# Kernel tuning notes

Hardware: AMD Instinct MI355X
Metric: run time of the kernel (lower is better)

The kernel has to match this reference:

```python
import jax, jax.numpy as jnp
import numpy as np

B, T, D, L = 64, 512, 400, 25
H = D // 2  # per-direction LSTM hidden


def setup_inputs():
    key = jax.random.key(0)
    ks = jax.random.split(key, 16)
    s = 0.1
    lengths = jax.random.randint(ks[0], (B,), T // 2, T + 1)
    mask = (jnp.arange(T)[None, :] < lengths[:, None]).astype(jnp.float32)
    labels = (jax.random.randint(ks[1], (B, T), 1, L) * mask.astype(jnp.int32)).astype(jnp.int32)

    def n(k, shape):
        return jax.random.normal(k, shape, jnp.float32) * s

    return {
        "input_embed": jax.random.normal(ks[2], (B, T, D), jnp.float32),
        "mask": mask,
        "labels": labels,
        "Wih_f": n(ks[3], (4 * H, D)), "Whh_f": n(ks[4], (4 * H, H)),
        "bih_f": n(ks[5], (4 * H,)), "bhh_f": n(ks[6], (4 * H,)),
        "Wih_b": n(ks[7], (4 * H, D)), "Whh_b": n(ks[8], (4 * H, H)),
        "bih_b": n(ks[9], (4 * H,)), "bhh_b": n(ks[10], (4 * H,)),
        "Wl": n(ks[11], (L, D)), "bl": n(ks[12], (L,)),
        "trans": n(ks[13], (L, L)), "start": n(ks[14], (L,)), "end": n(ks[15], (L,)),
    }


def _lstm_dir(x_tbd, m_tb1, Wih, Whh, bih, bhh, reverse):
    # Masked LSTM scan == pack_padded semantics: state frozen past sequence end.
    Bn = x_tbd.shape[1]
    h0 = jnp.zeros((Bn, H), x_tbd.dtype)

    def step(carry, inp):
        h, c = carry
        x, m = inp
        g = x @ Wih.T + h @ Whh.T + (bih + bhh)
        i, f, gg, o = jnp.split(g, 4, axis=-1)  # PyTorch gate order i,f,g,o
        i, f, o = jax.nn.sigmoid(i), jax.nn.sigmoid(f), jax.nn.sigmoid(o)
        c_new = f * c + i * jnp.tanh(gg)
        h_new = o * jnp.tanh(c_new)
        h = m * h_new + (1.0 - m) * h
        c = m * c_new + (1.0 - m) * c
        return (h, c), h

    _, hs = jax.lax.scan(step, (h0, h0), (x_tbd, m_tb1), reverse=reverse)
    return hs  # [T,B,H]


def _emissions(input_embed, mask, params):
    (Wih_f, Whh_f, bih_f, bhh_f, Wih_b, Whh_b, bih_b, bhh_b, Wl, bl) = params
    x = jnp.transpose(input_embed, (1, 0, 2))    # [T,B,D]
    m = jnp.transpose(mask, (1, 0))[:, :, None]  # [T,B,1]
    hf = _lstm_dir(x, m, Wih_f, Whh_f, bih_f, bhh_f, False)
    hb = _lstm_dir(x, m, Wih_b, Whh_b, bih_b, bhh_b, True)
    h = jnp.concatenate([hf, hb], axis=-1) * m   # pad positions zeroed like pad_packed_sequence
    e = (h @ Wl.T + bl) * m                      # `out *= mask.unsqueeze(-1)`
    return jnp.transpose(e, (1, 0, 2))           # [B,T,L]


def _crf_llh(e, labels, mask, trans, start, end):
    # numerator (gold path score)
    em = jnp.take_along_axis(e, labels[..., None], axis=-1)[..., 0]  # [B,T]
    tr = trans[labels[:, :-1], labels[:, 1:]]                        # [B,T-1]
    last = (jnp.sum(mask, axis=1) - 1.0).astype(jnp.int32)
    y_last = jnp.take_along_axis(labels, last[:, None], axis=1)[:, 0]
    num = start[labels[:, 0]] + em[:, 0] \
        + jnp.sum(mask[:, 1:] * (em[:, 1:] + tr), axis=1) + end[y_last]
    # log-partition via forward algorithm
    e_t = jnp.transpose(e, (1, 0, 2))  # [T,B,L]
    m_t = jnp.transpose(mask, (1, 0))  # [T,B]
    alpha0 = start[None, :] + e_t[0]

    def step(alpha, inp):
        et, mt = inp
        new = jax.nn.logsumexp(alpha[:, :, None] + trans[None], axis=1) + et
        return jnp.where(mt[:, None] > 0, new, alpha), None

    alpha, _ = jax.lax.scan(step, alpha0, (e_t[1:], m_t[1:]))
    logZ = jax.nn.logsumexp(alpha + end[None, :], axis=-1)
    return num - logZ  # [B] log-likelihood


def _viterbi(e, mask, trans, start, end):
    Bn = e.shape[0]
    e_t = jnp.transpose(e, (1, 0, 2))
    m_t = jnp.transpose(mask, (1, 0))
    delta0 = start[None, :] + e_t[0]
    eye_idx = jnp.broadcast_to(jnp.arange(L, dtype=jnp.int32), (Bn, L))

    def step(delta, inp):
        et, mt = inp
        cand = delta[:, :, None] + trans[None]  # [B, L_prev, L_cur]
        ptr = jnp.argmax(cand, axis=1).astype(jnp.int32)
        new = jnp.max(cand, axis=1) + et
        mb = mt[:, None] > 0
        return jnp.where(mb, new, delta), jnp.where(mb, ptr, eye_idx)

    delta, ptrs = jax.lax.scan(step, delta0, (e_t[1:], m_t[1:]))  # ptrs: [T-1,B,L]
    y_last = jnp.argmax(delta + end[None, :], axis=-1).astype(jnp.int32)  # [B]

    def back(y, ptr):
        y_prev = jnp.take_along_axis(ptr, y[:, None], axis=1)[:, 0]
        return y_prev, y_prev

    _, ys = jax.lax.scan(back, y_last, ptrs, reverse=True)  # [T-1,B]
    path = jnp.concatenate([ys, y_last[None]], axis=0)      # [T,B]
    return jnp.transpose(path, (1, 0)) * mask.astype(jnp.int32)  # pads -> pad_idx 0


def reference(input_embed, mask, labels, Wih_f, Whh_f, bih_f, bhh_f,
              Wih_b, Whh_b, bih_b, bhh_b, Wl, bl, trans, start, end):
    params = (Wih_f, Whh_f, bih_f, bhh_f, Wih_b, Whh_b, bih_b, bhh_b, Wl, bl)
    e = _emissions(input_embed, mask, params)
    loss = -jnp.mean(_crf_llh(e, labels, mask, trans, start, end))  # -torch.mean(score)
    preds = _viterbi(e, mask, trans, start, end)
    return loss, preds
```

## Files before the change

kernel.cpp:

```cpp
#include <hip/hip_runtime.h>
#include <cmath>

#define Bn 64
#define Tn 512
#define Dn 400
#define Ln 25
#define Hn 200
#define G4n 800
#define TCn 64
#define NCH 8
#define NPADn 832
#define JV 20
#define JLB 17
#define JSB 3

constexpr size_t OFF_WIHT = 0;
constexpr size_t OFF_WHHP = OFF_WIHT + (size_t)2*Dn*NPADn;
constexpr size_t OFF_WHHB = OFF_WHHP + (size_t)2*Hn*G4n;
constexpr size_t OFF_BSUM = OFF_WHHB + (size_t)2*Hn*G4n/2;
constexpr size_t OFF_GB   = OFF_BSUM + (size_t)2*G4n;
constexpr size_t OFF_HCAT = OFF_GB + (size_t)2*2*Bn*TCn*G4n/2;
constexpr size_t OFF_E    = OFF_HCAT + (size_t)Bn*Tn*2*Hn;
constexpr size_t OFF_HST  = OFF_E + (size_t)Bn*Tn*Ln;
constexpr size_t OFF_CST  = OFF_HST + (size_t)2*Bn*Hn;
constexpr size_t OFF_PART = OFF_CST + (size_t)2*Bn*Hn;

#define SMEM_BYTES 153664

__device__ __forceinline__ float sigf(float x) { return 1.0f / (1.0f + expf(-x)); }
__device__ __forceinline__ float rdlane(float v, int j) {
    return __uint_as_float(__builtin_amdgcn_readlane(__float_as_uint(v), j));
}

__global__ void prep_kernel(const float* __restrict__ Wih_f, const float* __restrict__ Whh_f,
                            const float* __restrict__ bih_f, const float* __restrict__ bhh_f,
                            const float* __restrict__ Wih_b, const float* __restrict__ Whh_b,
                            const float* __restrict__ bih_b, const float* __restrict__ bhh_b,
                            float* __restrict__ ws) {
    int tid = blockIdx.x * blockDim.x + threadIdx.x;
    int nth = gridDim.x * blockDim.x;
    float* WihT = ws + OFF_WIHT;
    float* WhhP = ws + OFF_WHHP;
    unsigned short* WhhB = (unsigned short*)(ws + OFF_WHHB);
    float* bsum = ws + OFF_BSUM;
    float* hst  = ws + OFF_HST;
    float* cst  = ws + OFF_CST;
    for (int i = tid; i < 2*Dn*NPADn; i += nth) {
        int d = i / (Dn*NPADn); int r = i % (Dn*NPADn); int k = r / NPADn; int g = r % NPADn;
        const float* W = d ? Wih_b : Wih_f;
        WihT[i] = (g < G4n) ? W[(size_t)g*Dn + k] : 0.0f;
    }
    for (int i = tid; i < 2*Hn*G4n; i += nth) {
        int d = i / (Hn*G4n); int r = i % (Hn*G4n);
        int j = r / G4n; int g = r % G4n;
        int k = g >> 2, q = g & 3;
        const float* W = d ? Whh_b : Whh_f;
        float v = W[(size_t)(q*Hn + k)*Hn + j];
        WhhP[i] = v;
        WhhB[i] = (unsigned short)(__float_as_uint(v) >> 16);
    }
    for (int i = tid; i < 2*G4n; i += nth) {
        int d = i / G4n; int g = i % G4n;
        bsum[i] = d ? (bih_b[g] + bhh_b[g]) : (bih_f[g] + bhh_f[g]);
    }
    for (int i = tid; i < 2*Bn*Hn; i += nth) { hst[i] = 0.0f; cst[i] = 0.0f; }
}

__device__ __forceinline__ void gemm_role(const float* __restrict__ X, float* __restrict__ ws,
                                          int chunk, int tile, int tid, char* smem) {
    const float* WihT = ws + OFF_WIHT;
    const float* bsum = ws + OFF_BSUM;
    unsigned short* Gb = (unsigned short*)(ws + OFF_GB) + (size_t)(chunk & 1) * 2 * Bn * TCn * G4n;
    int q4 = tid >> 8;
    int t2 = tid & 255;
    float* As = (float*)(smem + q4 * 13056);
    float* Bs = As + 16 * 136;
    int g0i = tile % 13; int rem = tile / 13;
    int bp = rem % 32;   int d = rem / 32;
    int g0 = g0i * 64;
    int tx = t2 % 16, ty = t2 / 16;
    int t_base = (d == 0) ? chunk * TCn : (Tn - (chunk + 1) * TCn);
    const float* Bmat = WihT + (size_t)d * Dn * NPADn;

    float acc[8][4] = {{0.f}};
    int lr = t2 / 2, lk = t2 % 2;
    int bk = t2 / 16, bg = t2 % 16;
    int a_b = bp * 2 + lr / 64;
    int a_t = t_base + (lr % 64);
    const float* Arow = X + ((size_t)a_b * Tn + a_t) * Dn;

    for (int kt = 0; kt < Dn; kt += 16) {
        float4 a4a = *(const float4*)(Arow + kt + lk * 8);
        float4 a4b = *(const float4*)(Arow + kt + lk * 8 + 4);
        float4 b4  = *(const float4*)(Bmat + (size_t)(kt + bk) * NPADn + g0 + bg * 4);
        __syncthreads();
        As[(lk*8+0)*136 + lr] = a4a.x; As[(lk*8+1)*136 + lr] = a4a.y;
        As[(lk*8+2)*136 + lr] = a4a.z; As[(lk*8+3)*136 + lr] = a4a.w;
        As[(lk*8+4)*136 + lr] = a4b.x; As[(lk*8+5)*136 + lr] = a4b.y;
        As[(lk*8+6)*136 + lr] = a4b.z; As[(lk*8+7)*136 + lr] = a4b.w;
        *(float4*)&Bs[bk*68 + bg*4] = b4;
        __syncthreads();
        #pragma unroll
        for (int kk = 0; kk < 16; ++kk) {
            float4 af0 = *(const float4*)&As[kk*136 + ty*8];
            float4 af1 = *(const float4*)&As[kk*136 + ty*8 + 4];
            float4 bf  = *(const float4*)&Bs[kk*68 + tx*4];
            acc[0][0] += af0.x*bf.x; acc[0][1] += af0.x*bf.y; acc[0][2] += af0.x*bf.z; acc[0][3] += af0.x*bf.w;
            acc[1][0] += af0.y*bf.x; acc[1][1] += af0.y*bf.y; acc[1][2] += af0.y*bf.z; acc[1][3] += af0.y*bf.w;
            acc[2][0] += af0.z*bf.x; acc[2][1] += af0.z*bf.y; acc[2][2] += af0.z*bf.z; acc[2][3] += af0.z*bf.w;
            acc[3][0] += af0.w*bf.x; acc[3][1] += af0.w*bf.y; acc[3][2] += af0.w*bf.z; acc[3][3] += af0.w*bf.w;
            acc[4][0] += af1.x*bf.x; acc[4][1] += af1.x*bf.y; acc[4][2] += af1.x*bf.z; acc[4][3] += af1.x*bf.w;
            acc[5][0] += af1.y*bf.x; acc[5][1] += af1.y*bf.y; acc[5][2] += af1.y*bf.z; acc[5][3] += af1.y*bf.w;
            acc[6][0] += af1.z*bf.x; acc[6][1] += af1.z*bf.y; acc[6][2] += af1.z*bf.z; acc[6][3] += af1.z*bf.w;
            acc[7][0] += af1.w*bf.x; acc[7][1] += af1.w*bf.y; acc[7][2] += af1.w*bf.z; acc[7][3] += af1.w*bf.w;
        }
    }
    #pragma unroll
    for (int ii = 0; ii < 8; ++ii) {
        int r = ty * 8 + ii;
        int b = bp * 2 + r / 64;
        int tloc = r % 64;
        #pragma unroll
        for (int jj = 0; jj < 4; ++jj) {
            int g = g0 + tx * 4 + jj;
            if (g < G4n) {
                int k = g % Hn, q = g / Hn;
                float v = acc[ii][jj] + bsum[d*G4n + g];
                Gb[(((size_t)d*Bn + b)*TCn + tloc)*G4n + k*4 + q] =
                    (unsigned short)(__float_as_uint(v) >> 16);
            }
        }
    }
}

__device__ __forceinline__ void rec_role(const float* __restrict__ mask, float* __restrict__ ws,
                                         int chunk, int b, int d, int tid, char* smem) {
    const unsigned short* Gbs = (const unsigned short*)(ws + OFF_GB) + (size_t)(chunk & 1) * 2 * Bn * TCn * G4n;
    float* Hcat = ws + OFF_HCAT;
    float* hst = ws + OFF_HST;
    float* cst = ws + OFF_CST;
    const float* WP = ws + OFF_WHHP;
    const unsigned short* WBbase = (const unsigned short*)(ws + OFF_WHHB);

    uint2*  wldsB   = (uint2*)smem;
    float4* partial = (float4*)(smem + 136000);
    float*  hbuf    = (float*)(smem + 152000);

    int k = tid % 200;
    int part = tid / 200;
    bool act = (part < 5);
    int cbase = (act ? part : 0) * 40;
    int qq = tid & 3, kk = tid >> 2;
    bool bact = (tid < 800);

    const float* Wd = WP + (size_t)d * Hn * G4n;
    const unsigned short* WB = WBbase + (size_t)d * Hn * G4n;
    #define LW(i) float4 w##i = *(const float4*)(Wd + (size_t)(cbase + i) * G4n + k * 4);
    LW(0) LW(1) LW(2) LW(3) LW(4) LW(5) LW(6) LW(7) LW(8) LW(9)
    LW(10) LW(11) LW(12) LW(13) LW(14) LW(15) LW(16) LW(17) LW(18) LW(19)
    #undef LW
    int lbase = (act ? part : 0) * 200 + k;
    if (act) {
        #pragma unroll
        for (int jj = 0; jj < JLB; ++jj)
            wldsB[jj * 1000 + part * 200 + k] = *(const uint2*)(WB + (size_t)(cbase + JV + jj) * G4n + k * 4);
    }
    size_t soff = ((size_t)d * Bn + b) * Hn;
    float hr = 0.f, cr = 0.f;
    if (bact && qq == 0) {
        hr = hst[soff + kk];
        cr = cst[soff + kk];
    }
    if (tid < 200) hbuf[tid] = hst[soff + tid];
    __syncthreads();

    const unsigned short* WstB = WB + (size_t)(cbase + JV + JLB) * G4n + k * 4;
    const unsigned short* GbRow = Gbs + ((size_t)d * Bn + b) * TCn * G4n;
    const float* mrow = mask + (size_t)b * Tn;
    float* Hrow = Hcat + (size_t)b * Tn * (2 * Hn) + d * Hn;

    #define FMAB(U, H) { \
        float bx = __uint_as_float((U).x << 16); \
        float by = __uint_as_float((U).x & 0xffff0000u); \
        float bz = __uint_as_float((U).y << 16); \
        float bw = __uint_as_float((U).y & 0xffff0000u); \
        acc.x += bx*(H); acc.y += by*(H); acc.z += bz*(H); acc.w += bw*(H); }
    #define FMA1(W, H) acc.x += (W).x*(H); acc.y += (W).y*(H); acc.z += (W).z*(H); acc.w += (W).w*(H);

    int cur = 0;
    for (int s = 0; s < TCn; ++s) {
        int tg, tloc;
        if (d == 0) { tloc = s; tg = chunk * TCn + s; }
        else        { tloc = TCn - 1 - s; tg = Tn - 1 - (chunk * TCn + s); }
        if (s > 0 && tid < 200) {
            int tgp = (d == 0) ? (chunk * TCn + s - 1) : (Tn - 1 - (chunk * TCn + s - 1));
            Hrow[(size_t)tgp * (2 * Hn) + tid] = hbuf[cur * 208 + tid];
        }
        float m_ = 0.f, gq = 0.f;
        if (bact) {
            m_ = mrow[tg];
            unsigned short gub = GbRow[(size_t)tloc * G4n + tid];
            gq = __uint_as_float((unsigned int)gub << 16);
        }
        {
            uint2 t0 = *(const uint2*)(WstB + (size_t)0 * G4n);
            uint2 t1 = *(const uint2*)(WstB + (size_t)1 * G4n);
            uint2 t2s = *(const uint2*)(WstB + (size_t)2 * G4n);
            float4 acc = {0.f, 0.f, 0.f, 0.f};
            float4 hv;
            const float* hb = hbuf + cur * 208;
            hv = *(const float4*)&hb[cbase + 0];
            FMA1(w0, hv.x) FMA1(w1, hv.y) FMA1(w2, hv.z) FMA1(w3, hv.w)
            hv = *(const float4*)&hb[cbase + 4];
            FMA1(w4, hv.x) FMA1(w5, hv.y) FMA1(w6, hv.z) FMA1(w7, hv.w)
            hv = *(const float4*)&hb[cbase + 8];
            FMA1(w8, hv.x) FMA1(w9, hv.y) FMA1(w10, hv.z) FMA1(w11, hv.w)
            hv = *(const float4*)&hb[cbase + 12];
            FMA1(w12, hv.x) FMA1(w13, hv.y) FMA1(w14, hv.z) FMA1(w15, hv.w)
            hv = *(const float4*)&hb[cbase + 16];
            FMA1(w16, hv.x) FMA1(w17, hv.y) FMA1(w18, hv.z) FMA1(w19, hv.w)
            {
                uint2 u0 = wldsB[0*1000+lbase], u1 = wldsB[1*1000+lbase];
                uint2 u2 = wldsB[2*1000+lbase], u3 = wldsB[3*1000+lbase];
                hv = *(const float4*)&hb[cbase + 20];
                FMAB(u0, hv.x) FMAB(u1, hv.y) FMAB(u2, hv.z) FMAB(u3, hv.w)
            }
            {
                uint2 u0 = wldsB[4*1000+lbase], u1 = wldsB[5*1000+lbase];
                uint2 u2 = wldsB[6*1000+lbase], u3 = wldsB[7*1000+lbase];
                hv = *(const float4*)&hb[cbase + 24];
                FMAB(u0, hv.x) FMAB(u1, hv.y) FMAB(u2, hv.z) FMAB(u3, hv.w)
            }
            {
                uint2 u0 = wldsB[8*1000+lbase], u1 = wldsB[9*1000+lbase];
                uint2 u2 = wldsB[10*1000+lbase], u3 = wldsB[11*1000+lbase];
                hv = *(const float4*)&hb[cbase + 28];
                FMAB(u0, hv.x) FMAB(u1, hv.y) FMAB(u2, hv.z) FMAB(u3, hv.w)
            }
            {
                uint2 u0 = wldsB[12*1000+lbase], u1 = wldsB[13*1000+lbase];
                uint2 u2 = wldsB[14*1000+lbase], u3 = wldsB[15*1000+lbase];
                hv = *(const float4*)&hb[cbase + 32];
                FMAB(u0, hv.x) FMAB(u1, hv.y) FMAB(u2, hv.z) FMAB(u3, hv.w)
            }
            {
                uint2 u16 = wldsB[16*1000+lbase];
                hv = *(const float4*)&hb[cbase + 36];
                FMAB(u16, hv.x) FMAB(t0, hv.y) FMAB(t1, hv.z) FMAB(t2s, hv.w)
            }
            if (act) partial[part * 200 + k] = acc;
        }
        __syncthreads();
        if (bact) {
            const float* pf = (const float*)partial;
            float g = gq + (((pf[0*800 + tid] + pf[1*800 + tid]) +
                             (pf[2*800 + tid] + pf[3*800 + tid])) + pf[4*800 + tid]);
            float arg = (qq == 2) ? 2.f * g : g;
            float sg = 1.f / (1.f + expf(-arg));
            float a = (qq == 2) ? 2.f * sg - 1.f : sg;
            float x1 = __shfl_xor(a, 1);
            float x2 = __shfl_xor(a, 2);
            float x3 = __shfl_xor(x1, 2);
            if (qq == 0) {
                float i_ = a, f_ = x1, gg_ = x2, o_ = x3;
                float cn = f_ * cr + i_ * gg_;
                float hn = o_ * tanhf(cn);
                cr = m_ * cn + (1.f - m_) * cr;
                hr = m_ * hn + (1.f - m_) * hr;
                hbuf[(cur ^ 1) * 208 + kk] = hr;
            }
        }
        __syncthreads();
        cur ^= 1;
    }
    #undef FMAB
    #undef FMA1
    if (tid < 200) {
        int tgp = (d == 0) ? (chunk * TCn + TCn - 1) : (Tn - 1 - (chunk * TCn + TCn - 1));
        Hrow[(size_t)tgp * (2 * Hn) + tid] = hbuf[cur * 208 + tid];
    }
    if (bact && qq == 0) {
        hst[soff + kk] = hr;
        cst[soff + kk] = cr;
    }
}

__global__ __launch_bounds__(1024, 4) void fused_kernel(const float* __restrict__ X,
                                                        const float* __restrict__ mask,
                                                        float* __restrict__ ws,
                                                        int rec_chunk, int gemm_chunk, int nrec) {
    __shared__ __align__(16) char smem[SMEM_BYTES];
    int bx = blockIdx.x;
    int tid = threadIdx.x;
    if (bx < nrec) {
        rec_role(mask, ws, rec_chunk, bx & 63, bx >> 6, tid, smem);
    } else {
        int tile = (bx - nrec) * 4 + (tid >> 8);
        gemm_role(X, ws, gemm_chunk, tile, tid, smem);
    }
}

__global__ __launch_bounds__(256) void emis_kernel(const float* __restrict__ mask,
                                                   const float* __restrict__ Wl,
                                                   const float* __restrict__ bl,
                                                   float* __restrict__ ws) {
    const float* Hcat = ws + OFF_HCAT;
    float* E = ws + OFF_E;
    __shared__ float Wls[Ln * 404];
    __shared__ float Hs[16 * 404];
    int tid = threadIdx.x;
    for (int i = tid; i < Ln * 100; i += 256) {
        int l = i / 100, k4 = i % 100;
        *(float4*)&Wls[l*404 + k4*4] = *(const float4*)(Wl + (size_t)l*Dn + k4*4);
    }
    int rbase = blockIdx.x * 128;
    for (int sub = 0; sub < 8; ++sub) {
        int r0 = rbase + sub * 16;
        __syncthreads();
        for (int i = tid; i < 16 * 100; i += 256) {
            int r = i / 100, k4 = i % 100;
            *(float4*)&Hs[r*404 + k4*4] = *(const float4*)(Hcat + (size_t)(r0 + r)*Dn + k4*4);
        }
        __syncthreads();
        for (int o = tid; o < 16 * Ln; o += 256) {
            int r = o / Ln, l = o % Ln;
            float acc = 0.f;
            #pragma unroll 4
            for (int k4 = 0; k4 < 100; ++k4) {
                float4 h = *(const float4*)&Hs[r*404 + k4*4];
                float4 wv = *(const float4*)&Wls[l*404 + k4*4];
                acc += h.x*wv.x + h.y*wv.y + h.z*wv.z + h.w*wv.w;
            }
            int row = r0 + r;
            float m = mask[row];
            E[(size_t)row * Ln + l] = (acc + bl[l]) * m;
        }
    }
}

__global__ __launch_bounds__(128) void decode_kernel(const float* __restrict__ mask,
                                                     const int* __restrict__ labels,
                                                     const float* __restrict__ trans,
                                                     const float* __restrict__ start,
                                                     const float* __restrict__ endv,
                                                     float* __restrict__ ws,
                                                     float* __restrict__ out) {
    int b = blockIdx.x;
    int tid = threadIdx.x;
    int wvid = tid >> 6;
    int l = tid & 63;
    const float* E = ws + OFF_E;
    float* part = ws + OFF_PART;

    __shared__ __align__(16) float Es[Tn * Ln];
    __shared__ float trs[Ln * Ln];
    __shared__ unsigned char ptrs[Tn][Ln];
    __shared__ unsigned char ys[Tn];

    {
        const float4* src = (const float4*)(E + (size_t)b * Tn * Ln);
        float4* dst = (float4*)Es;
        for (int i = tid; i < Tn * Ln / 4; i += 128) dst[i] = src[i];
        for (int i = tid; i < Ln * Ln; i += 128) trs[i] = trans[i];
    }
    float cnt = 0.f;
    for (int t = l; t < Tn; t += 64) cnt += mask[(size_t)b * Tn + t];
    for (int off = 32; off; off >>= 1) cnt += __shfl_xor(cnt, off);
    int len = (int)(cnt + 0.5f);
    float trc[Ln];
    #pragma unroll
    for (int j = 0; j < Ln; ++j) trc[j] = -1e30f;
    if (l < Ln) {
        #pragma unroll
        for (int j = 0; j < Ln; ++j) trc[j] = trans[j * Ln + l];
    }
    __syncthreads();

    if (wvid == 0) {
        float alpha = (l < Ln) ? start[l] + Es[l] : -1e30f;
        for (int t = 1; t < len; ++t) {
            float v[Ln];
            #pragma unroll
            for (int j = 0; j < Ln; ++j) v[j] = rdlane(alpha, j) + trc[j];
            float r[12];
            #pragma unroll
            for (int j = 0; j < 12; ++j) r[j] = fmaxf(v[j], v[j + 12]);
            r[0] = fmaxf(r[0], v[24]);
            #pragma unroll
            for (int j = 0; j < 6; ++j) r[j] = fmaxf(r[j], r[j + 6]);
            #pragma unroll
            for (int j = 0; j < 3; ++j) r[j] = fmaxf(r[j], r[j + 3]);
            float mx = fmaxf(fmaxf(r[0], r[1]), r[2]);
            float e[Ln];
            #pragma unroll
            for (int j = 0; j < Ln; ++j) e[j] = __expf(v[j] - mx);
            #pragma unroll
            for (int j = 0; j < 12; ++j) e[j] += e[j + 12];
            e[0] += e[24];
            #pragma unroll
            for (int j = 0; j < 6; ++j) e[j] += e[j + 6];
            #pragma unroll
            for (int j = 0; j < 3; ++j) e[j] += e[j + 3];
            float s = (e[0] + e[1]) + e[2];
            float nv = mx + __logf(s) + Es[t * Ln + l];
            alpha = (l < Ln) ? nv : -1e30f;
        }
        float vfin = (l < Ln) ? alpha + endv[l] : -1e30f;
        float mxf = vfin;
        for (int off = 32; off; off >>= 1) mxf = fmaxf(mxf, __shfl_xor(mxf, off));
        float sf = (l < Ln) ? __expf(vfin - mxf) : 0.f;
        for (int off = 32; off; off >>= 1) sf += __shfl_xor(sf, off);
        float logZ = mxf + __logf(sf);
        float psum = 0.f;
        for (int t = l; t < len; t += 64) {
            if (t >= 1) {
                int lt = labels[(size_t)b * Tn + t];
                int lp = labels[(size_t)b * Tn + t - 1];
                psum += Es[t * Ln + lt] + trs[lp * Ln + lt];
            }
        }
        for (int off = 32; off; off >>= 1) psum += __shfl_xor(psum, off);
        if (l == 0) {
            int l0 = labels[(size_t)b * Tn];
            int yl = labels[(size_t)b * Tn + len - 1];
            part[b] = start[l0] + Es[l0] + psum + endv[yl] - logZ;
        }
    } else {
        float delta = (l < Ln) ? start[l] + Es[l] : -1e30f;
        for (int t = 1; t < len; ++t) {
            float best = -1e30f; int ba = 0;
            #pragma unroll
            for (int j = 0; j < Ln; ++j) {
                float c = rdlane(delta, j) + trc[j];
                if (c > best) { best = c; ba = j; }
            }
            float nd = best + Es[t * Ln + l];
            if (l < Ln) ptrs[t][l] = (unsigned char)ba;
            delta = (l < Ln) ? nd : -1e30f;
        }
        float bb = -1e30f; int y = 0;
        #pragma unroll
        for (int j = 0; j < Ln; ++j) {
            float c = rdlane(delta, j) + endv[j];
            if (c > bb) { bb = c; y = j; }
        }
        if (l == 0) {
            ys[len - 1] = (unsigned char)y;
            int yy = y;
            for (int t = len - 1; t >= 1; --t) { yy = ptrs[t][yy]; ys[t - 1] = (unsigned char)yy; }
        }
        for (int t = l; t < Tn; t += 64) {
            out[1 + (size_t)b * Tn + t] = (t < len) ? (float)ys[t] : 0.f;
        }
    }
}

__global__ __launch_bounds__(64) void fin_kernel(float* __restrict__ ws, float* __restrict__ out) {
    const float* part = ws + OFF_PART;
    int l = threadIdx.x;
    float v = (l < Bn) ? part[l] : 0.f;
    for (int off = 32; off; off >>= 1) v += __shfl_xor(v, off);
    if (l == 0) out[0] = -v / (float)Bn;
}

extern "C" void kernel_launch(void* const* d_in, const int* in_sizes, int n_in,
                              void* d_out, int out_size, void* d_ws, size_t ws_size,
                              hipStream_t stream) {
    (void)in_sizes; (void)n_in; (void)out_size; (void)ws_size;
    const float* X      = (const float*)d_in[0];
    const float* mask   = (const float*)d_in[1];
    const int*   labels = (const int*)d_in[2];
    const float* Wih_f  = (const float*)d_in[3];
    const float* Whh_f  = (const float*)d_in[4];
    const float* bih_f  = (const float*)d_in[5];
    const float* bhh_f  = (const float*)d_in[6];
    const float* Wih_b  = (const float*)d_in[7];
    const float* Whh_b  = (const float*)d_in[8];
    const float* bih_b  = (const float*)d_in[9];
    const float* bhh_b  = (const float*)d_in[10];
    const float* Wl     = (const float*)d_in[11];
    const float* bl     = (const float*)d_in[12];
    const float* trans  = (const float*)d_in[13];
    const float* start  = (const float*)d_in[14];
    const float* endv   = (const float*)d_in[15];
    float* ws  = (float*)d_ws;
    float* out = (float*)d_out;

    prep_kernel<<<128, 256, 0, stream>>>(Wih_f, Whh_f, bih_f, bhh_f,
                                         Wih_b, Whh_b, bih_b, bhh_b, ws);
    fused_kernel<<<208, 1024, 0, stream>>>(X, mask, ws, 0, 0, 0);
    for (int c = 1; c < NCH; ++c)
        fused_kernel<<<336, 1024, 0, stream>>>(X, mask, ws, c - 1, c, 128);
    fused_kernel<<<128, 1024, 0, stream>>>(X, mask, ws, NCH - 1, 0, 128);
    emis_kernel<<<256, 256, 0, stream>>>(mask, Wl, bl, ws);
    decode_kernel<<<64, 128, 0, stream>>>(mask, labels, trans, start, endv, ws, out);
    fin_kernel<<<1, 64, 0, stream>>>(ws, out);
}
```

Measured before the change: 2.122 ms.

## Overlap emission GEMM with last recurrence chunk; split CRF decode across half-waves

Adds an emission role to the fused kernel. In the final launch, extra blocks compute emissions for the middle time rows (64..447), whose forward and backward hidden states are already final, while the last recurrence chunk runs. A smaller follow-up kernel handles the remaining edge rows. The CRF forward and Viterbi loops now split the 25 predecessor labels across the two 32-lane halves of a wave, using shuffles and a cross-half combine, which shortens the serial per-step dependency chain. This adds shuffle overhead and role-dispatch complexity, and relies on hidden states for middle rows being complete before the last chunk.

After: 2.136 ms. No clear change (+0.7%).

```diff
diff --git a/kernel.cpp b/kernel.cpp
--- a/kernel.cpp
+++ b/kernel.cpp
@@ -28,9 +28,6 @@
 #define SMEM_BYTES 153664
 
 __device__ __forceinline__ float sigf(float x) { return 1.0f / (1.0f + expf(-x)); }
-__device__ __forceinline__ float rdlane(float v, int j) {
-    return __uint_as_float(__builtin_amdgcn_readlane(__float_as_uint(v), j));
-}
 
 __global__ void prep_kernel(const float* __restrict__ Wih_f, const float* __restrict__ Whh_f,
                             const float* __restrict__ bih_f, const float* __restrict__ bhh_f,
@@ -285,37 +282,82 @@
     }
 }
 
+__device__ __forceinline__ void emis_role(const float* __restrict__ mask,
+                                          const float* __restrict__ Wl, const float* __restrict__ bl,
+                                          float* __restrict__ ws, int blk, int tid, char* smem) {
+    const float* Hcat = ws + OFF_HCAT;
+    float* E = ws + OFF_E;
+    float* Wls = (float*)smem;
+    int q4 = tid >> 8, t2 = tid & 255;
+    float* Hs = (float*)(smem + 40448 + q4 * 25856);
+    for (int i = tid; i < Ln * 100; i += 1024) {
+        int l = i / 100, k4 = i % 100;
+        *(float4*)&Wls[l*404 + k4*4] = *(const float4*)(Wl + (size_t)l*Dn + k4*4);
+    }
+    int Q = blk * 4 + q4;
+    int b = Q / 3, seg = Q % 3;
+    int rbase = b * Tn + 64 + seg * 128;
+    for (int sub = 0; sub < 8; ++sub) {
+        int r0 = rbase + sub * 16;
+        __syncthreads();
+        for (int i = t2; i < 16 * 100; i += 256) {
+            int r = i / 100, k4 = i % 100;
+            *(float4*)&Hs[r*404 + k4*4] = *(const float4*)(Hcat + (size_t)(r0 + r)*Dn + k4*4);
+        }
+        __syncthreads();
+        for (int o = t2; o < 16 * Ln; o += 256) {
+            int r = o / Ln, l = o % Ln;
+            float acc = 0.f;
+            #pragma unroll 4
+            for (int k4 = 0; k4 < 100; ++k4) {
+                float4 h = *(const float4*)&Hs[r*404 + k4*4];
+                float4 wv = *(const float4*)&Wls[l*404 + k4*4];
+                acc += h.x*wv.x + h.y*wv.y + h.z*wv.z + h.w*wv.w;
+            }
+            int row = r0 + r;
+            float m = mask[row];
+            E[(size_t)row * Ln + l] = (acc + bl[l]) * m;
+        }
+    }
+}
+
 __global__ __launch_bounds__(1024, 4) void fused_kernel(const float* __restrict__ X,
                                                         const float* __restrict__ mask,
+                                                        const float* __restrict__ Wl,
+                                                        const float* __restrict__ bl,
                                                         float* __restrict__ ws,
-                                                        int rec_chunk, int gemm_chunk, int nrec) {
+                                                        int rec_chunk, int gemm_chunk,
+                                                        int nrec, int ngemm) {
     __shared__ __align__(16) char smem[SMEM_BYTES];
     int bx = blockIdx.x;
     int tid = threadIdx.x;
     if (bx < nrec) {
         rec_role(mask, ws, rec_chunk, bx & 63, bx >> 6, tid, smem);
-    } else {
+    } else if (bx < nrec + ngemm) {
         int tile = (bx - nrec) * 4 + (tid >> 8);
         gemm_role(X, ws, gemm_chunk, tile, tid, smem);
-    }
-}
-
-__global__ __launch_bounds__(256) void emis_kernel(const float* __restrict__ mask,
-                                                   const float* __restrict__ Wl,
-                                                   const float* __restrict__ bl,
-                                                   float* __restrict__ ws) {
+    } else {
+        emis_role(mask, Wl, bl, ws, bx - nrec - ngemm, tid, smem);
+    }
+}
+
+__global__ __launch_bounds__(256) void emis2_kernel(const float* __restrict__ mask,
+                                                    const float* __restrict__ Wl,
+                                                    const float* __restrict__ bl,
+                                                    float* __restrict__ ws) {
     const float* Hcat = ws + OFF_HCAT;
     float* E = ws + OFF_E;
     __shared__ float Wls[Ln * 404];
     __shared__ float Hs[16 * 404];
     int tid = threadIdx.x;
+    int b = blockIdx.x;
     for (int i = tid; i < Ln * 100; i += 256) {
         int l = i / 100, k4 = i % 100;
         *(float4*)&Wls[l*404 + k4*4] = *(const float4*)(Wl + (size_t)l*Dn + k4*4);
     }
-    int rbase = blockIdx.x * 128;
     for (int sub = 0; sub < 8; ++sub) {
-        int r0 = rbase + sub * 16;
+        int t0 = (sub < 4) ? sub * 16 : 448 + (sub - 4) * 16;
+        int r0 = b * Tn + t0;
         __syncthreads();
         for (int i = tid; i < 16 * 100; i += 256) {
             int r = i / 100, k4 = i % 100;
@@ -348,7 +390,12 @@
     int b = blockIdx.x;
     int tid = threadIdx.x;
     int wvid = tid >> 6;
-    int l = tid & 63;
+    int ln = tid & 63;
+    int half = (ln >> 5) & 1;
+    int l = ln & 31;
+    bool actl = (l < Ln);
+    int jbase = half ? 13 : 0;
+    int jcnt  = half ? 12 : 13;
     const float* E = ws + OFF_E;
     float* part = ws + OFF_PART;
 
@@ -364,55 +411,50 @@
         for (int i = tid; i < Ln * Ln; i += 128) trs[i] = trans[i];
     }
     float cnt = 0.f;
-    for (int t = l; t < Tn; t += 64) cnt += mask[(size_t)b * Tn + t];
+    for (int t = ln; t < Tn; t += 64) cnt += mask[(size_t)b * Tn + t];
     for (int off = 32; off; off >>= 1) cnt += __shfl_xor(cnt, off);
     int len = (int)(cnt + 0.5f);
-    float trc[Ln];
+    float trc[13];
     #pragma unroll
-    for (int j = 0; j < Ln; ++j) trc[j] = -1e30f;
-    if (l < Ln) {
-        #pragma unroll
-        for (int j = 0; j < Ln; ++j) trc[j] = trans[j * Ln + l];
+    for (int j = 0; j < 13; ++j) trc[j] = -1e30f;
+    if (actl) {
+        for (int j = 0; j < jcnt; ++j) trc[j] = trans[(jbase + j) * Ln + l];
     }
     __syncthreads();
 
     if (wvid == 0) {
-        float alpha = (l < Ln) ? start[l] + Es[l] : -1e30f;
+        float alpha = actl ? start[l] + Es[l] : -1e30f;
         for (int t = 1; t < len; ++t) {
-            float v[Ln];
+            float v[13];
             #pragma unroll
-            for (int j = 0; j < Ln; ++j) v[j] = rdlane(alpha, j) + trc[j];
-            float r[12];
+            for (int j = 0; j < 13; ++j) v[j] = __shfl(alpha, jbase + j) + trc[j];
+            float a0 = fmaxf(v[0], v[1]), a1 = fmaxf(v[2], v[3]), a2 = fmaxf(v[4], v[5]);
+            float a3 = fmaxf(v[6], v[7]), a4 = fmaxf(v[8], v[9]), a5 = fmaxf(v[10], v[11]);
+            a0 = fmaxf(a0, a1); a2 = fmaxf(a2, a3); a4 = fmaxf(a4, a5);
+            a0 = fmaxf(a0, a2); a4 = fmaxf(a4, v[12]);
+            float m = fmaxf(a0, a4);
+            float e[13];
             #pragma unroll
-            for (int j = 0; j < 12; ++j) r[j] = fmaxf(v[j], v[j + 12]);
-            r[0] = fmaxf(r[0], v[24]);
-            #pragma unroll
-            for (int j = 0; j < 6; ++j) r[j] = fmaxf(r[j], r[j + 6]);
-            #pragma unroll
-            for (int j = 0; j < 3; ++j) r[j] = fmaxf(r[j], r[j + 3]);
-            float mx = fmaxf(fmaxf(r[0], r[1]), r[2]);
-            float e[Ln];
-            #pragma unroll
-            for (int j = 0; j < Ln; ++j) e[j] = __expf(v[j] - mx);
-            #pragma unroll
-            for (int j = 0; j < 12; ++j) e[j] += e[j + 12];
-            e[0] += e[24];
-            #pragma unroll
-            for (int j = 0; j < 6; ++j) e[j] += e[j + 6];
-            #pragma unroll
-            for (int j = 0; j < 3; ++j) e[j] += e[j + 3];
-            float s = (e[0] + e[1]) + e[2];
-            float nv = mx + __logf(s) + Es[t * Ln + l];
-            alpha = (l < Ln) ? nv : -1e30f;
-        }
-        float vfin = (l < Ln) ? alpha + endv[l] : -1e30f;
+            for (int j = 0; j < 13; ++j) e[j] = __expf(v[j] - m);
+            float s0 = (e[0] + e[1]) + (e[2] + e[3]);
+            float s1 = (e[4] + e[5]) + (e[6] + e[7]);
+            float s2 = (e[8] + e[9]) + (e[10] + e[11]);
+            float s = ((s0 + s1) + (s2 + e[12]));
+            float pm = __shfl_xor(m, 32);
+            float ps = __shfl_xor(s, 32);
+            float M = fmaxf(m, pm);
+            float S = s * __expf(m - M) + ps * __expf(pm - M);
+            float nv = M + __logf(S) + Es[t * Ln + l];
+            alpha = actl ? nv : -1e30f;
+        }
+        float vfin = (ln < Ln) ? alpha + endv[l] : -1e30f;
         float mxf = vfin;
         for (int off = 32; off; off >>= 1) mxf = fmaxf(mxf, __shfl_xor(mxf, off));
-        float sf = (l < Ln) ? __expf(vfin - mxf) : 0.f;
+        float sf = (ln < Ln) ? __expf(vfin - mxf) : 0.f;
         for (int off = 32; off; off >>= 1) sf += __shfl_xor(sf, off);
         float logZ = mxf + __logf(sf);
         float psum = 0.f;
-        for (int t = l; t < len; t += 64) {
+        for (int t = ln; t < len; t += 64) {
             if (t >= 1) {
                 int lt = labels[(size_t)b * Tn + t];
                 int lp = labels[(size_t)b * Tn + t - 1];
@@ -420,36 +462,42 @@
             }
         }
         for (int off = 32; off; off >>= 1) psum += __shfl_xor(psum, off);
-        if (l == 0) {
+        if (ln == 0) {
             int l0 = labels[(size_t)b * Tn];
             int yl = labels[(size_t)b * Tn + len - 1];
             part[b] = start[l0] + Es[l0] + psum + endv[yl] - logZ;
         }
     } else {
-        float delta = (l < Ln) ? start[l] + Es[l] : -1e30f;
+        float delta = actl ? start[l] + Es[l] : -1e30f;
         for (int t = 1; t < len; ++t) {
             float best = -1e30f; int ba = 0;
             #pragma unroll
-            for (int j = 0; j < Ln; ++j) {
-                float c = rdlane(delta, j) + trc[j];
-                if (c > best) { best = c; ba = j; }
-            }
-            float nd = best + Es[t * Ln + l];
-            if (l < Ln) ptrs[t][l] = (unsigned char)ba;
-            delta = (l < Ln) ? nd : -1e30f;
+            for (int j = 0; j < 13; ++j) {
+                float c = __shfl(delta, jbase + j) + trc[j];
+                if (c > best) { best = c; ba = jbase + j; }
+            }
+            float pb = __shfl_xor(best, 32);
+            int   pa = __shfl_xor(ba, 32);
+            float b0 = half ? pb : best; int a0 = half ? pa : ba;
+            float b1 = half ? best : pb; int a1 = half ? ba : pa;
+            int   A  = (b1 > b0) ? a1 : a0;
+            float B  = fmaxf(b0, b1);
+            float nd = B + Es[t * Ln + l];
+            if (actl && half == 0) ptrs[t][l] = (unsigned char)A;
+            delta = actl ? nd : -1e30f;
         }
         float bb = -1e30f; int y = 0;
-        #pragma unroll
         for (int j = 0; j < Ln; ++j) {
-            float c = rdlane(delta, j) + endv[j];
+            float c = __shfl(delta, j) + endv[j];
             if (c > bb) { bb = c; y = j; }
         }
-        if (l == 0) {
+        if (ln == 0) {
             ys[len - 1] = (unsigned char)y;
             int yy = y;
             for (int t = len - 1; t >= 1; --t) { yy = ptrs[t][yy]; ys[t - 1] = (unsigned char)yy; }
         }
-        for (int t = l; t < Tn; t += 64) {
+        __builtin_amdgcn_s_barrier();
+        for (int t = ln; t < Tn; t += 64) {
             out[1 + (size_t)b * Tn + t] = (t < len) ? (float)ys[t] : 0.f;
         }
     }
@@ -488,11 +536,11 @@
 
     prep_kernel<<<128, 256, 0, stream>>>(Wih_f, Whh_f, bih_f, bhh_f,
                                          Wih_b, Whh_b, bih_b, bhh_b, ws);
-    fused_kernel<<<208, 1024, 0, stream>>>(X, mask, ws, 0, 0, 0);
+    fused_kernel<<<208, 1024, 0, stream>>>(X, mask, Wl, bl, ws, 0, 0, 0, 208);
     for (int c = 1; c < NCH; ++c)
-        fused_kernel<<<336, 1024, 0, stream>>>(X, mask, ws, c - 1, c, 128);
-    fused_kernel<<<128, 1024, 0, stream>>>(X, mask, ws, NCH - 1, 0, 128);
-    emis_kernel<<<256, 256, 0, stream>>>(mask, Wl, bl, ws);
+        fused_kernel<<<336, 1024, 0, stream>>>(X, mask, Wl, bl, ws, c - 1, c, 128, 208);
+    fused_kernel<<<176, 1024, 0, stream>>>(X, mask, Wl, bl, ws, NCH - 1, 0, 128, 0);
+    emis2_kernel<<<64, 256, 0, stream>>>(mask, Wl, bl, ws);
     decode_kernel<<<64, 128, 0, stream>>>(mask, labels, trans, start, endv, ws, out);
     fin_kernel<<<1, 64, 0, stream>>>(ws, out);
 }
```
